# Optimization experiments

Measured on AMD Instinct MI355X. Metric: run time of the kernel, lower is better.

## Reference

```python
import jax, jax.numpy as jnp
import numpy as np
import math

B, L, HD, H = 4, 1024, 512, 8
D = HD // H  # 64 per-head dim


def setup_inputs() -> dict:
    key = jax.random.key(0)
    ks = jax.random.split(key, 9)
    query = jax.random.normal(ks[0], (B, L, HD), jnp.float32)
    key_ = jax.random.normal(ks[1], (B, L, HD), jnp.float32)
    value = jax.random.normal(ks[2], (B, L, HD), jnp.float32)
    kernel = jax.random.normal(ks[3], (B * H, L, L), jnp.float32) * 0.1
    # sparse-ish boolean mask; low density so no row is fully masked
    attn_mask = jax.random.bernoulli(ks[4], 0.05, (B * H, L, L))
    in_proj_weight = jax.random.normal(ks[5], (3 * HD, HD), jnp.float32) * 0.02
    in_proj_bias = jnp.zeros((3 * HD,), jnp.float32)
    out_w = jax.random.normal(ks[6], (HD, HD), jnp.float32) * 0.02
    out_b = jnp.zeros((HD,), jnp.float32)
    return dict(query=query, key_=key_, value=value, attn_mask=attn_mask,
                key_padding_mask=0, kernel=kernel,
                in_proj_weight=in_proj_weight, in_proj_bias=in_proj_bias,
                out_w=out_w, out_b=out_b)


def _split_heads(x):
    # [B, L, HD] -> [B*H, L, D]
    b, l, _ = x.shape
    return x.reshape(b, l, H, D).transpose(0, 2, 1, 3).reshape(b * H, l, D)


def _merge_heads(x):
    # [B*H, L, D] -> [B, L, HD]
    bh, l, d = x.shape
    b = bh // H
    return x.reshape(b, H, l, d).transpose(0, 2, 1, 3).reshape(b, l, H * d)


def reference(query, key_, value, attn_mask, key_padding_mask, kernel,
              in_proj_weight, in_proj_bias, out_w, out_b):
    # key_padding_mask is falsy (None-equivalent) -> attn_mask unchanged
    wq, wk, wv = in_proj_weight[:HD], in_proj_weight[HD:2 * HD], in_proj_weight[2 * HD:]
    bq, bk, bv = in_proj_bias[:HD], in_proj_bias[HD:2 * HD], in_proj_bias[2 * HD:]
    q = _split_heads(query @ wq.T + bq)   # [B*H, L, D]
    k = _split_heads(key_ @ wk.T + bk)
    v = _split_heads(value @ wv.T + bv)
    scale = 1.0 / math.sqrt(D)
    scores = jnp.einsum('bqd,bkd->bqk', q, k) * scale  # [B*H, Lq, Lk]
    scores = scores + kernel.transpose(0, 2, 1)        # additive kernel bias
    scores = jnp.where(attn_mask, -jnp.inf, scores)    # masked_fill
    attn = jax.nn.softmax(scores, axis=-1)
    out = jnp.einsum('bqk,bkd->bqd', attn, v)          # [B*H, Lq, D]
    out = _merge_heads(out)                            # [B, Lq, HD]
    return out @ out_w.T + out_b
```

## Files before the change

### kernel.cpp

```cpp
#include <hip/hip_runtime.h>
#include <hip/hip_bf16.h>
#include <cstdint>
#include <cstddef>

typedef _Float16 half8 __attribute__((ext_vector_type(8)));
typedef float f32x4 __attribute__((ext_vector_type(4)));

#define NB 4
#define NL 1024
#define NHD 512
#define NH 8
#define ND 64
#define NBH 32

#define MFMA16(a, b, c) __builtin_amdgcn_mfma_f32_16x16x32_f16((a), (b), (c), 0, 0, 0)

__global__ void detect_mask_kernel(const unsigned int* __restrict__ m, int* __restrict__ flag) {
    __shared__ int s_byte;
    if (threadIdx.x == 0) s_byte = 0;
    __syncthreads();
    int bad = 0;
    for (int i = threadIdx.x; i < 16384; i += 256) {
        unsigned int w = m[i];
        if (w != 0u && w != 1u && w != 0x3F800000u) bad = 1;
    }
    if (bad) atomicOr(&s_byte, 1);
    __syncthreads();
    if (threadIdx.x == 0) *flag = s_byte;
}

__global__ __launch_bounds__(256) void bitmask_kernel(
    const void* __restrict__ mask, const int* __restrict__ flagp, unsigned* __restrict__ mb)
{
    const int t = blockIdx.x * 256 + threadIdx.x;
    unsigned w = 0;
    if (*flagp == 1) {
        const uint4* p = (const uint4*)((const unsigned char*)mask + (size_t)t * 32);
        uint4 a = p[0], b = p[1];
        unsigned src[8] = {a.x, a.y, a.z, a.w, b.x, b.y, b.z, b.w};
#pragma unroll
        for (int j = 0; j < 8; ++j) {
            unsigned u = src[j];
            w |= ((u & 0x000000FFu) ? 1u : 0u) << (4 * j + 0);
            w |= ((u & 0x0000FF00u) ? 1u : 0u) << (4 * j + 1);
            w |= ((u & 0x00FF0000u) ? 1u : 0u) << (4 * j + 2);
            w |= ((u & 0xFF000000u) ? 1u : 0u) << (4 * j + 3);
        }
    } else {
        const uint4* p = (const uint4*)((const unsigned*)mask + (size_t)t * 32);
#pragma unroll
        for (int j = 0; j < 8; ++j) {
            uint4 v = p[j];
            w |= (v.x ? 1u : 0u) << (4 * j + 0);
            w |= (v.y ? 1u : 0u) << (4 * j + 1);
            w |= (v.z ? 1u : 0u) << (4 * j + 2);
            w |= (v.w ? 1u : 0u) << (4 * j + 3);
        }
    }
    mb[t] = w;
}

__global__ __launch_bounds__(256) void qkv_gemm_kernel(
    const float* __restrict__ qin, const float* __restrict__ kin, const float* __restrict__ vin,
    const float* __restrict__ w, const float* __restrict__ bias,
    _Float16* __restrict__ qb, _Float16* __restrict__ kb, _Float16* __restrict__ vtb)
{
    const int mtile = blockIdx.x, ntile = blockIdx.y, proj = blockIdx.z;
    const float* A = proj == 0 ? qin : (proj == 1 ? kin : vin);
    const float* W = w + (size_t)proj * NHD * NHD;

    __shared__ __align__(16) _Float16 a_lds[64][72];
    __shared__ __align__(16) _Float16 b_lds[64][72];

    const int tid = threadIdx.x;
    const int wave = tid >> 6, lane = tid & 63, quad = lane >> 4, c = lane & 15;
    const int wm = wave >> 1, wn = wave & 1;

    f32x4 acc[2][2] = {};

    const int sr = tid >> 2, sc = (tid & 3) * 16;
    const float* pa = &A[(size_t)(mtile * 64 + sr) * NHD + sc];
    const float* pb = &W[(size_t)(ntile * 64 + sr) * NHD + sc];

    f32x4 ar[4], br[4];
#pragma unroll
    for (int j = 0; j < 4; ++j) { ar[j] = *(const f32x4*)(pa + j * 4); br[j] = *(const f32x4*)(pb + j * 4); }

    for (int k0 = 0; k0 < NHD; k0 += 64) {
        half8 ah0, ah1, bh0, bh1;
#pragma unroll
        for (int j = 0; j < 4; ++j) {
            ah0[j] = (_Float16)ar[0][j]; ah0[4 + j] = (_Float16)ar[1][j];
            ah1[j] = (_Float16)ar[2][j]; ah1[4 + j] = (_Float16)ar[3][j];
            bh0[j] = (_Float16)br[0][j]; bh0[4 + j] = (_Float16)br[1][j];
            bh1[j] = (_Float16)br[2][j]; bh1[4 + j] = (_Float16)br[3][j];
        }
        __syncthreads();
        *(half8*)&a_lds[sr][sc] = ah0; *(half8*)&a_lds[sr][sc + 8] = ah1;
        *(half8*)&b_lds[sr][sc] = bh0; *(half8*)&b_lds[sr][sc + 8] = bh1;
        if (k0 < NHD - 64) {
            const float* na = pa + k0 + 64;
            const float* nb = pb + k0 + 64;
#pragma unroll
            for (int j = 0; j < 4; ++j) { ar[j] = *(const f32x4*)(na + j * 4); br[j] = *(const f32x4*)(nb + j * 4); }
        }
        __syncthreads();

#pragma unroll
        for (int kk = 0; kk < 2; ++kk) {
            half8 af0 = *(const half8*)&a_lds[wm * 32 + c][kk * 32 + quad * 8];
            half8 af1 = *(const half8*)&a_lds[wm * 32 + 16 + c][kk * 32 + quad * 8];
            half8 bf0 = *(const half8*)&b_lds[wn * 32 + c][kk * 32 + quad * 8];
            half8 bf1 = *(const half8*)&b_lds[wn * 32 + 16 + c][kk * 32 + quad * 8];
            acc[0][0] = MFMA16(af0, bf0, acc[0][0]);
            acc[0][1] = MFMA16(af0, bf1, acc[0][1]);
            acc[1][0] = MFMA16(af1, bf0, acc[1][0]);
            acc[1][1] = MFMA16(af1, bf1, acc[1][1]);
        }
    }

#pragma unroll
    for (int ms = 0; ms < 2; ++ms)
#pragma unroll
    for (int ns = 0; ns < 2; ++ns) {
        const int Cc = ntile * 64 + wn * 32 + ns * 16 + c;
        const float bv = bias[proj * NHD + Cc];
        const int h = Cc >> 6, d = Cc & 63;
#pragma unroll
        for (int r = 0; r < 4; ++r) {
            const int R = mtile * 64 + wm * 32 + ms * 16 + quad * 4 + r;
            const int b = R >> 10, l = R & 1023;
            const int bh = b * NH + h;
            float val = acc[ms][ns][r] + bv;
            if (proj == 0) {
                qb[((size_t)(bh * NL + l)) * ND + d] = (_Float16)(val * 0.125f);
            } else if (proj == 1) {
                kb[((size_t)(bh * NL + l)) * ND + d] = (_Float16)val;
            } else {
                vtb[((size_t)(bh * ND + d)) * NL + l] = (_Float16)val;
            }
        }
    }
}

__global__ __launch_bounds__(256) void attn_kernel(
    const _Float16* __restrict__ qb, const _Float16* __restrict__ kb, const _Float16* __restrict__ vtb,
    const float* __restrict__ kern, const unsigned* __restrict__ mb,
    _Float16* __restrict__ ctx)
{
    const int qt = blockIdx.x, bh = blockIdx.y;
    const int tid = threadIdx.x, wave = tid >> 6, lane = tid & 63, quad = lane >> 4, c = lane & 15;
    const int q_base = qt * 64 + wave * 16;

    __shared__ __align__(16) _Float16 k_lds[64][72];
    __shared__ __align__(16) _Float16 vt_lds[64][72];
    __shared__ __align__(16) _Float16 p_lds[64][72];
    __shared__ __align__(16) float bias_lds[64][68];
    __shared__ unsigned mask_lds[64][2];

    half8 aq0 = *(const half8*)&qb[((size_t)(bh * NL) + q_base + c) * ND + quad * 8];
    half8 aq1 = *(const half8*)&qb[((size_t)(bh * NL) + q_base + c) * ND + 32 + quad * 8];

    f32x4 O[4] = {};
    float m_i[4] = {-1e30f, -1e30f, -1e30f, -1e30f};
    float l_i[4] = {0.f, 0.f, 0.f, 0.f};

    const int sr = tid >> 2, sc = (tid & 3) * 16;

    half8 kr0, kr1, vr0, vr1;
    f32x4 gr[4];
    unsigned mr = 0;

    {
        const _Float16* pk = &kb[((size_t)(bh * NL) + sr) * ND + sc];
        kr0 = *(const half8*)pk; kr1 = *(const half8*)(pk + 8);
        const _Float16* pv = &vtb[((size_t)(bh * ND) + sr) * NL + sc];
        vr0 = *(const half8*)pv; vr1 = *(const half8*)(pv + 8);
        const float* pg = &kern[((size_t)bh * NL + sr) * NL + qt * 64 + sc];
#pragma unroll
        for (int j = 0; j < 4; ++j) gr[j] = *(const f32x4*)(pg + j * 4);
        if (tid < 128) mr = mb[((size_t)bh * NL + qt * 64 + (tid >> 1)) * 32 + (tid & 1)];
    }

    for (int kt = 0; kt < 16; ++kt) {
        __syncthreads();
        *(half8*)&k_lds[sr][sc] = kr0;  *(half8*)&k_lds[sr][sc + 8] = kr1;
        *(half8*)&vt_lds[sr][sc] = vr0; *(half8*)&vt_lds[sr][sc + 8] = vr1;
#pragma unroll
        for (int j = 0; j < 4; ++j) *(f32x4*)&bias_lds[sr][(tid & 3) * 16 + j * 4] = gr[j];
        if (tid < 128) mask_lds[tid >> 1][tid & 1] = mr;

        if (kt < 15) {
            const int ktn = kt + 1;
            const _Float16* pk = &kb[((size_t)(bh * NL) + ktn * 64 + sr) * ND + sc];
            kr0 = *(const half8*)pk; kr1 = *(const half8*)(pk + 8);
            const _Float16* pv = &vtb[((size_t)(bh * ND) + sr) * NL + ktn * 64 + sc];
            vr0 = *(const half8*)pv; vr1 = *(const half8*)(pv + 8);
            const float* pg = &kern[((size_t)bh * NL + ktn * 64 + sr) * NL + qt * 64 + sc];
#pragma unroll
            for (int j = 0; j < 4; ++j) gr[j] = *(const f32x4*)(pg + j * 4);
            if (tid < 128) mr = mb[((size_t)bh * NL + qt * 64 + (tid >> 1)) * 32 + ktn * 2 + (tid & 1)];
        }
        __syncthreads();

        f32x4 S[4];
#pragma unroll
        for (int ns = 0; ns < 4; ++ns) {
            f32x4 a = {};
            half8 bk0 = *(const half8*)&k_lds[ns * 16 + c][quad * 8];
            half8 bk1 = *(const half8*)&k_lds[ns * 16 + c][32 + quad * 8];
            a = MFMA16(aq0, bk0, a);
            a = MFMA16(aq1, bk1, a);
            S[ns] = a;
        }

        unsigned mw0[4], mw1[4];
#pragma unroll
        for (int r = 0; r < 4; ++r) {
            const int row = wave * 16 + quad * 4 + r;
            uint2 mm = *(const uint2*)&mask_lds[row][0];
            mw0[r] = mm.x; mw1[r] = mm.y;
        }

#pragma unroll
        for (int ns = 0; ns < 4; ++ns) {
            f32x4 bv = *(const f32x4*)&bias_lds[ns * 16 + c][wave * 16 + quad * 4];
            const int bit = ((ns & 1) << 4) + c;
#pragma unroll
            for (int r = 0; r < 4; ++r) {
                unsigned w = (ns < 2) ? mw0[r] : mw1[r];
                bool mk = (w >> bit) & 1u;
                S[ns][r] = mk ? -1e30f : (S[ns][r] + bv[r]);
            }
        }

        float pm[4], al[4];
#pragma unroll
        for (int r = 0; r < 4; ++r) {
            float t = fmaxf(fmaxf(S[0][r], S[1][r]), fmaxf(S[2][r], S[3][r]));
            t = fmaxf(t, __shfl_xor(t, 1));
            t = fmaxf(t, __shfl_xor(t, 2));
            t = fmaxf(t, __shfl_xor(t, 4));
            t = fmaxf(t, __shfl_xor(t, 8));
            float mn = fmaxf(m_i[r], t);
            al[r] = __expf(m_i[r] - mn);
            m_i[r] = mn;
            pm[r] = mn;
        }
        float rs[4] = {0.f, 0.f, 0.f, 0.f};
#pragma unroll
        for (int ns = 0; ns < 4; ++ns)
#pragma unroll
            for (int r = 0; r < 4; ++r) {
                float p = __expf(S[ns][r] - pm[r]);
                S[ns][r] = p;
                rs[r] += p;
            }
#pragma unroll
        for (int r = 0; r < 4; ++r) {
            float t = rs[r];
            t += __shfl_xor(t, 1);
            t += __shfl_xor(t, 2);
            t += __shfl_xor(t, 4);
            t += __shfl_xor(t, 8);
            l_i[r] = l_i[r] * al[r] + t;
        }
#pragma unroll
        for (int ds = 0; ds < 4; ++ds)
#pragma unroll
            for (int r = 0; r < 4; ++r)
                O[ds][r] *= al[r];

#pragma unroll
        for (int ns = 0; ns < 4; ++ns)
#pragma unroll
            for (int r = 0; r < 4; ++r)
                p_lds[wave * 16 + quad * 4 + r][ns * 16 + c] = (_Float16)S[ns][r];
        __asm__ volatile("s_waitcnt lgkmcnt(0)" ::: "memory");

#pragma unroll
        for (int ks = 0; ks < 2; ++ks) {
            half8 ap = *(const half8*)&p_lds[wave * 16 + c][ks * 32 + quad * 8];
#pragma unroll
            for (int ds = 0; ds < 4; ++ds) {
                half8 bv = *(const half8*)&vt_lds[ds * 16 + c][ks * 32 + quad * 8];
                O[ds] = MFMA16(ap, bv, O[ds]);
            }
        }
    }

    const int b = bh >> 3, h = bh & 7;
#pragma unroll
    for (int ds = 0; ds < 4; ++ds) {
        const int d = ds * 16 + c;
#pragma unroll
        for (int r = 0; r < 4; ++r) {
            const int qg = q_base + quad * 4 + r;
            float val = O[ds][r] / l_i[r];
            ctx[((size_t)(b * NL + qg)) * NHD + h * ND + d] = (_Float16)val;
        }
    }
}

__global__ __launch_bounds__(256) void out_gemm_kernel(
    const _Float16* __restrict__ ctx, const float* __restrict__ w, const float* __restrict__ bias,
    float* __restrict__ out)
{
    const int mtile = blockIdx.x, ntile = blockIdx.y;
    __shared__ __align__(16) _Float16 a_lds[64][72];
    __shared__ __align__(16) _Float16 b_lds[64][72];
    const int tid = threadIdx.x, wave = tid >> 6, lane = tid & 63, quad = lane >> 4, c = lane & 15;
    const int wm = wave >> 1, wn = wave & 1;
    f32x4 acc[2][2] = {};

    const int sr = tid >> 2, sc = (tid & 3) * 16;
    const _Float16* pa = &ctx[(size_t)(mtile * 64 + sr) * NHD + sc];
    const float* pb = &w[(size_t)(ntile * 64 + sr) * NHD + sc];

    half8 ah0, ah1;
    f32x4 br[4];
    ah0 = *(const half8*)pa; ah1 = *(const half8*)(pa + 8);
#pragma unroll
    for (int j = 0; j < 4; ++j) br[j] = *(const f32x4*)(pb + j * 4);

    for (int k0 = 0; k0 < NHD; k0 += 64) {
        half8 bh0, bh1;
#pragma unroll
        for (int j = 0; j < 4; ++j) {
            bh0[j] = (_Float16)br[0][j]; bh0[4 + j] = (_Float16)br[1][j];
            bh1[j] = (_Float16)br[2][j]; bh1[4 + j] = (_Float16)br[3][j];
        }
        __syncthreads();
        *(half8*)&a_lds[sr][sc] = ah0; *(half8*)&a_lds[sr][sc + 8] = ah1;
        *(half8*)&b_lds[sr][sc] = bh0; *(half8*)&b_lds[sr][sc + 8] = bh1;
        if (k0 < NHD - 64) {
            const _Float16* na = pa + k0 + 64;
            const float* nb = pb + k0 + 64;
            ah0 = *(const half8*)na; ah1 = *(const half8*)(na + 8);
#pragma unroll
            for (int j = 0; j < 4; ++j) br[j] = *(const f32x4*)(nb + j * 4);
        }
        __syncthreads();

#pragma unroll
        for (int kk = 0; kk < 2; ++kk) {
            half8 af0 = *(const half8*)&a_lds[wm * 32 + c][kk * 32 + quad * 8];
            half8 af1 = *(const half8*)&a_lds[wm * 32 + 16 + c][kk * 32 + quad * 8];
            half8 bf0 = *(const half8*)&b_lds[wn * 32 + c][kk * 32 + quad * 8];
            half8 bf1 = *(const half8*)&b_lds[wn * 32 + 16 + c][kk * 32 + quad * 8];
            acc[0][0] = MFMA16(af0, bf0, acc[0][0]);
            acc[0][1] = MFMA16(af0, bf1, acc[0][1]);
            acc[1][0] = MFMA16(af1, bf0, acc[1][0]);
            acc[1][1] = MFMA16(af1, bf1, acc[1][1]);
        }
    }

#pragma unroll
    for (int ms = 0; ms < 2; ++ms)
#pragma unroll
    for (int ns = 0; ns < 2; ++ns) {
        const int Cc = ntile * 64 + wn * 32 + ns * 16 + c;
        const float bv = bias[Cc];
#pragma unroll
        for (int r = 0; r < 4; ++r) {
            const int R = mtile * 64 + wm * 32 + ms * 16 + quad * 4 + r;
            out[(size_t)R * NHD + Cc] = acc[ms][ns][r] + bv;
        }
    }
}

extern "C" void kernel_launch(void* const* d_in, const int* in_sizes, int n_in,
                              void* d_out, int out_size, void* d_ws, size_t ws_size,
                              hipStream_t stream)
{
    const float* query = (const float*)d_in[0];
    const float* key_  = (const float*)d_in[1];
    const float* value = (const float*)d_in[2];
    const void*  mask  = d_in[3];
    const float* kern  = (const float*)d_in[5];
    const float* ipw   = (const float*)d_in[6];
    const float* ipb   = (const float*)d_in[7];
    const float* outw  = (const float*)d_in[8];
    const float* outb  = (const float*)d_in[9];

    char* ws = (char*)d_ws;
    _Float16* qb  = (_Float16*)(ws);
    _Float16* kb  = (_Float16*)(ws + (4ull << 20));
    _Float16* vtb = (_Float16*)(ws + (8ull << 20));
    _Float16* ctx = (_Float16*)(ws + (12ull << 20));
    int* flag     = (int*)(ws + (16ull << 20));

    unsigned* mb = (unsigned*)d_out;

    detect_mask_kernel<<<1, 256, 0, stream>>>((const unsigned int*)mask, flag);
    bitmask_kernel<<<4096, 256, 0, stream>>>(mask, flag, mb);
    qkv_gemm_kernel<<<dim3(64, 8, 3), 256, 0, stream>>>(query, key_, value, ipw, ipb, qb, kb, vtb);
    attn_kernel<<<dim3(16, 32), 256, 0, stream>>>(qb, kb, vtb, kern, mb, ctx);
    out_gemm_kernel<<<dim3(64, 8), 256, 0, stream>>>(ctx, outw, outb, (float*)d_out);
}
```

Before: 394.8 us.

## Split attention over key halves and merge partial softmax results

```diff
diff --git a/kernel.cpp b/kernel.cpp
--- a/kernel.cpp
+++ b/kernel.cpp
@@ -4,6 +4,7 @@
 #include <cstddef>
 
 typedef _Float16 half8 __attribute__((ext_vector_type(8)));
+typedef _Float16 half4 __attribute__((ext_vector_type(4)));
 typedef float f32x4 __attribute__((ext_vector_type(4)));
 
 #define NB 4
@@ -15,14 +16,20 @@
 
 #define MFMA16(a, b, c) __builtin_amdgcn_mfma_f32_16x16x32_f16((a), (b), (c), 0, 0, 0)
 
-__global__ void detect_mask_kernel(const unsigned int* __restrict__ m, int* __restrict__ flag) {
+__global__ void detect_mask_kernel(const uint4* __restrict__ m, int* __restrict__ flag) {
     __shared__ int s_byte;
     if (threadIdx.x == 0) s_byte = 0;
     __syncthreads();
+    uint4 v[4];
+#pragma unroll
+    for (int j = 0; j < 4; ++j) v[j] = m[threadIdx.x * 4 + j];
     int bad = 0;
-    for (int i = threadIdx.x; i < 16384; i += 256) {
-        unsigned int w = m[i];
-        if (w != 0u && w != 1u && w != 0x3F800000u) bad = 1;
+#pragma unroll
+    for (int j = 0; j < 4; ++j) {
+        unsigned ws[4] = {v[j].x, v[j].y, v[j].z, v[j].w};
+#pragma unroll
+        for (int i = 0; i < 4; ++i)
+            if (ws[i] != 0u && ws[i] != 1u && ws[i] != 0x3F800000u) bad = 1;
     }
     if (bad) atomicOr(&s_byte, 1);
     __syncthreads();
@@ -146,11 +153,12 @@
 __global__ __launch_bounds__(256) void attn_kernel(
     const _Float16* __restrict__ qb, const _Float16* __restrict__ kb, const _Float16* __restrict__ vtb,
     const float* __restrict__ kern, const unsigned* __restrict__ mb,
-    _Float16* __restrict__ ctx)
-{
-    const int qt = blockIdx.x, bh = blockIdx.y;
+    float* __restrict__ pO, float* __restrict__ pm, float* __restrict__ pl)
+{
+    const int qt = blockIdx.x, bh = blockIdx.y, half = blockIdx.z;
     const int tid = threadIdx.x, wave = tid >> 6, lane = tid & 63, quad = lane >> 4, c = lane & 15;
     const int q_base = qt * 64 + wave * 16;
+    const int kt0 = half * 8;
 
     __shared__ __align__(16) _Float16 k_lds[64][72];
     __shared__ __align__(16) _Float16 vt_lds[64][72];
@@ -172,17 +180,17 @@
     unsigned mr = 0;
 
     {
-        const _Float16* pk = &kb[((size_t)(bh * NL) + sr) * ND + sc];
+        const _Float16* pk = &kb[((size_t)(bh * NL) + kt0 * 64 + sr) * ND + sc];
         kr0 = *(const half8*)pk; kr1 = *(const half8*)(pk + 8);
-        const _Float16* pv = &vtb[((size_t)(bh * ND) + sr) * NL + sc];
+        const _Float16* pv = &vtb[((size_t)(bh * ND) + sr) * NL + kt0 * 64 + sc];
         vr0 = *(const half8*)pv; vr1 = *(const half8*)(pv + 8);
-        const float* pg = &kern[((size_t)bh * NL + sr) * NL + qt * 64 + sc];
+        const float* pg = &kern[((size_t)bh * NL + kt0 * 64 + sr) * NL + qt * 64 + sc];
 #pragma unroll
         for (int j = 0; j < 4; ++j) gr[j] = *(const f32x4*)(pg + j * 4);
-        if (tid < 128) mr = mb[((size_t)bh * NL + qt * 64 + (tid >> 1)) * 32 + (tid & 1)];
-    }
-
-    for (int kt = 0; kt < 16; ++kt) {
+        if (tid < 128) mr = mb[((size_t)bh * NL + qt * 64 + (tid >> 1)) * 32 + kt0 * 2 + (tid & 1)];
+    }
+
+    for (int kt = 0; kt < 8; ++kt) {
         __syncthreads();
         *(half8*)&k_lds[sr][sc] = kr0;  *(half8*)&k_lds[sr][sc + 8] = kr1;
         *(half8*)&vt_lds[sr][sc] = vr0; *(half8*)&vt_lds[sr][sc + 8] = vr1;
@@ -190,16 +198,16 @@
         for (int j = 0; j < 4; ++j) *(f32x4*)&bias_lds[sr][(tid & 3) * 16 + j * 4] = gr[j];
         if (tid < 128) mask_lds[tid >> 1][tid & 1] = mr;
 
-        if (kt < 15) {
-            const int ktn = kt + 1;
-            const _Float16* pk = &kb[((size_t)(bh * NL) + ktn * 64 + sr) * ND + sc];
+        if (kt < 7) {
+            const int ktg = kt0 + kt + 1;
+            const _Float16* pk = &kb[((size_t)(bh * NL) + ktg * 64 + sr) * ND + sc];
             kr0 = *(const half8*)pk; kr1 = *(const half8*)(pk + 8);
-            const _Float16* pv = &vtb[((size_t)(bh * ND) + sr) * NL + ktn * 64 + sc];
+            const _Float16* pv = &vtb[((size_t)(bh * ND) + sr) * NL + ktg * 64 + sc];
             vr0 = *(const half8*)pv; vr1 = *(const half8*)(pv + 8);
-            const float* pg = &kern[((size_t)bh * NL + ktn * 64 + sr) * NL + qt * 64 + sc];
+            const float* pg = &kern[((size_t)bh * NL + ktg * 64 + sr) * NL + qt * 64 + sc];
 #pragma unroll
             for (int j = 0; j < 4; ++j) gr[j] = *(const f32x4*)(pg + j * 4);
-            if (tid < 128) mr = mb[((size_t)bh * NL + qt * 64 + (tid >> 1)) * 32 + ktn * 2 + (tid & 1)];
+            if (tid < 128) mr = mb[((size_t)bh * NL + qt * 64 + (tid >> 1)) * 32 + ktg * 2 + (tid & 1)];
         }
         __syncthreads();
 
@@ -234,7 +242,7 @@
             }
         }
 
-        float pm[4], al[4];
+        float pmax[4], al[4];
 #pragma unroll
         for (int r = 0; r < 4; ++r) {
             float t = fmaxf(fmaxf(S[0][r], S[1][r]), fmaxf(S[2][r], S[3][r]));
@@ -245,14 +253,14 @@
             float mn = fmaxf(m_i[r], t);
             al[r] = __expf(m_i[r] - mn);
             m_i[r] = mn;
-            pm[r] = mn;
+            pmax[r] = mn;
         }
         float rs[4] = {0.f, 0.f, 0.f, 0.f};
 #pragma unroll
         for (int ns = 0; ns < 4; ++ns)
 #pragma unroll
             for (int r = 0; r < 4; ++r) {
-                float p = __expf(S[ns][r] - pm[r]);
+                float p = __expf(S[ns][r] - pmax[r]);
                 S[ns][r] = p;
                 rs[r] += p;
             }
@@ -289,16 +297,54 @@
         }
     }
 
+    const int ub = (bh * 16 + qt) * 2 + half;
+    float* pOb = pO + (size_t)ub * 4096;
+#pragma unroll
+    for (int ds = 0; ds < 4; ++ds)
+#pragma unroll
+        for (int r = 0; r < 4; ++r)
+            pOb[(wave * 16 + quad * 4 + r) * 64 + ds * 16 + c] = O[ds][r];
+    if (c == 0) {
+#pragma unroll
+        for (int r = 0; r < 4; ++r) {
+            const int row = wave * 16 + quad * 4 + r;
+            pm[(size_t)ub * 64 + row] = m_i[r];
+            pl[(size_t)ub * 64 + row] = l_i[r];
+        }
+    }
+}
+
+__global__ __launch_bounds__(256) void merge_kernel(
+    const float* __restrict__ pO, const float* __restrict__ pm, const float* __restrict__ pl,
+    _Float16* __restrict__ ctx)
+{
+    const int qt = blockIdx.x, bh = blockIdx.y;
+    const int u0 = (bh * 16 + qt) * 2, u1 = u0 + 1;
+    __shared__ float s0[64], s1[64];
+    const int tid = threadIdx.x;
+    if (tid < 64) {
+        float m0 = pm[(size_t)u0 * 64 + tid], m1 = pm[(size_t)u1 * 64 + tid];
+        float l0 = pl[(size_t)u0 * 64 + tid], l1 = pl[(size_t)u1 * 64 + tid];
+        float m = fmaxf(m0, m1);
+        float e0 = __expf(m0 - m), e1 = __expf(m1 - m);
+        float linv = 1.0f / (l0 * e0 + l1 * e1);
+        s0[tid] = e0 * linv; s1[tid] = e1 * linv;
+    }
+    __syncthreads();
+    const float* O0 = pO + (size_t)u0 * 4096;
+    const float* O1 = pO + (size_t)u1 * 4096;
     const int b = bh >> 3, h = bh & 7;
 #pragma unroll
-    for (int ds = 0; ds < 4; ++ds) {
-        const int d = ds * 16 + c;
-#pragma unroll
-        for (int r = 0; r < 4; ++r) {
-            const int qg = q_base + quad * 4 + r;
-            float val = O[ds][r] / l_i[r];
-            ctx[((size_t)(b * NL + qg)) * NHD + h * ND + d] = (_Float16)val;
-        }
+    for (int j = 0; j < 4; ++j) {
+        const int idx = j * 1024 + tid * 4;
+        const int row = idx >> 6, col = idx & 63;
+        f32x4 a = *(const f32x4*)(O0 + idx);
+        f32x4 bb = *(const f32x4*)(O1 + idx);
+        const float sa = s0[row], sb = s1[row];
+        half4 o;
+#pragma unroll
+        for (int i = 0; i < 4; ++i) o[i] = (_Float16)(a[i] * sa + bb[i] * sb);
+        *(half4*)&ctx[((size_t)(b * NL + qt * 64 + row)) * NHD + h * ND + col] = o;
     }
 }
 
@@ -389,12 +435,16 @@
     _Float16* vtb = (_Float16*)(ws + (8ull << 20));
     _Float16* ctx = (_Float16*)(ws + (12ull << 20));
     int* flag     = (int*)(ws + (16ull << 20));
+    float* pO     = (float*)(ws + (24ull << 20));
+    float* pm     = (float*)(ws + (40ull << 20));
+    float* pl     = (float*)(ws + (41ull << 20));
 
     unsigned* mb = (unsigned*)d_out;
 
-    detect_mask_kernel<<<1, 256, 0, stream>>>((const unsigned int*)mask, flag);
+    detect_mask_kernel<<<1, 256, 0, stream>>>((const uint4*)mask, flag);
     bitmask_kernel<<<4096, 256, 0, stream>>>(mask, flag, mb);
     qkv_gemm_kernel<<<dim3(64, 8, 3), 256, 0, stream>>>(query, key_, value, ipw, ipb, qb, kb, vtb);
-    attn_kernel<<<dim3(16, 32), 256, 0, stream>>>(qb, kb, vtb, kern, mb, ctx);
+    attn_kernel<<<dim3(16, 32, 2), 256, 0, stream>>>(qb, kb, vtb, kern, mb, pO, pm, pl);
+    merge_kernel<<<dim3(16, 32), 256, 0, stream>>>(pO, pm, pl, ctx);
     out_gemm_kernel<<<dim3(64, 8), 256, 0, stream>>>(ctx, outw, outb, (float*)d_out);
 }
```

After: 370.6 us. 1.07x faster.
